# Kernel optimization log

Measured on AMD Instinct MI355X. Metric: run time of the kernel, lower is better.

The kernel has to match this reference:

```python
import jax, jax.numpy as jnp
import numpy as np

N_HEAD = 16
LN_EPS = 1e-5


def setup_inputs() -> dict:
    key = jax.random.key(0)
    ks = jax.random.split(key, 12)
    B, S, D = 4, 1024, 1024
    s = 1.0 / np.sqrt(D)
    return {
        "Q": jax.random.normal(ks[0], (B, S, D), jnp.float32),
        "K": jax.random.normal(ks[1], (B, S, D), jnp.float32),
        "V": jax.random.normal(ks[2], (B, S, D), jnp.float32),
        # Linear weights stored torch-style [out, in]
        "Wq": jax.random.normal(ks[3], (D, D), jnp.float32) * s,
        "bq": jnp.zeros((D,), jnp.float32),
        "Wk": jax.random.normal(ks[4], (D, D), jnp.float32) * s,
        "bk": jnp.zeros((D,), jnp.float32),
        "Wv": jax.random.normal(ks[5], (D, D), jnp.float32) * s,
        "bv": jnp.zeros((D,), jnp.float32),
        "Wo": jax.random.normal(ks[6], (D, D), jnp.float32) * s,
        "bo": jnp.zeros((D,), jnp.float32),
        "ln_g": jnp.ones((D,), jnp.float32),
        "ln_b": jnp.zeros((D,), jnp.float32),
    }


def _layer_norm(x, g, b):
    mu = jnp.mean(x, axis=-1, keepdims=True)
    var = jnp.mean(jnp.square(x - mu), axis=-1, keepdims=True)
    return (x - mu) * jax.lax.rsqrt(var + LN_EPS) * g + b


def reference(Q, K, V, Wq, bq, Wk, bk, Wv, bv, Wo, bo, ln_g, ln_b):
    B, S, D = Q.shape
    H = N_HEAD
    dk = D // H
    # projections, split heads: [B, H, S, dk]
    q = (Q @ Wq.T + bq).reshape(B, S, H, dk).transpose(0, 2, 1, 3)
    k = (K @ Wk.T + bk).reshape(B, S, H, dk).transpose(0, 2, 1, 3)
    v = (V @ Wv.T + bv).reshape(B, S, H, dk).transpose(0, 2, 1, 3)
    scores = jnp.einsum("bhqd,bhkd->bhqk", q, k) / np.sqrt(dk)
    # NOTE: original module applies softmax twice (F.softmax then nn.Softmax)
    attn = jax.nn.softmax(jax.nn.softmax(scores, axis=-1), axis=-1)
    ctx = jnp.einsum("bhqk,bhkd->bhqd", attn, v)  # [B, H, S, dk]
    ctx = ctx.transpose(0, 2, 1, 3).reshape(B, S, D)
    out = ctx @ Wo.T + bo
    return _layer_norm(out + Q, ln_g, ln_b)
```

## Files before the change

### kernel.cpp

```cpp
#include <hip/hip_runtime.h>
#include <cstdint>
#include <cstddef>


typedef unsigned short ushort_t;
typedef __attribute__((ext_vector_type(8))) short bf16x8;
typedef __attribute__((ext_vector_type(8))) unsigned short us8;
typedef __attribute__((ext_vector_type(4))) unsigned short us4;
typedef __attribute__((ext_vector_type(4))) float f32x4;

#define MFMA16(a, b, c) __builtin_amdgcn_mfma_f32_16x16x32_bf16((a), (b), (c), 0, 0, 0)
#define EXP2F(x) __builtin_amdgcn_exp2f(x)
#define LOG2E 1.4426950408889634f

__device__ __forceinline__ float b2f(ushort_t u) {
  union { unsigned int i; float f; } x; x.i = ((unsigned int)u) << 16; return x.f;
}
__device__ __forceinline__ ushort_t f2b(float f) {
  union { unsigned int i; float f; } x; x.f = f;
  unsigned int r = (x.i + 0x7FFFu + ((x.i >> 16) & 1u)) >> 16;
  return (ushort_t)r;
}
__device__ __forceinline__ us8 cvt8(float4 a, float4 b) {
  us8 r;
  r[0] = f2b(a.x); r[1] = f2b(a.y); r[2] = f2b(a.z); r[3] = f2b(a.w);
  r[4] = f2b(b.x); r[5] = f2b(b.y); r[6] = f2b(b.z); r[7] = f2b(b.w);
  return r;
}

__device__ __forceinline__ void gll16(const ushort_t* g, ushort_t* l) {
  __builtin_amdgcn_global_load_lds(
      (const __attribute__((address_space(1))) void*)g,
      (__attribute__((address_space(3))) void*)l, 16, 0, 0);
}

__global__ __launch_bounds__(256, 8) void cvt4_kernel(
    const float* __restrict__ w0, const float* __restrict__ w1,
    const float* __restrict__ w2, const float* __restrict__ w3,
    ushort_t* __restrict__ dst) {
  const int which = blockIdx.y;
  const float* src = (which == 0) ? w0 : (which == 1) ? w1 : (which == 2) ? w2 : w3;
  const int i = (blockIdx.x * 256 + threadIdx.x) * 8;
  const float4 a = *(const float4*)(src + i);
  const float4 b = *(const float4*)(src + i + 4);
  *(us8*)(dst + (size_t)which * 1048576 + i) = cvt8(a, b);
}

__global__ __launch_bounds__(256, 3) void qkv_proj_kernel(
    const float* __restrict__ Qin, const float* __restrict__ Kin,
    const float* __restrict__ Vin,
    const ushort_t* __restrict__ wq, const ushort_t* __restrict__ wk,
    const ushort_t* __restrict__ wv,
    const float* __restrict__ bq, const float* __restrict__ bk,
    const float* __restrict__ bv,
    ushort_t* __restrict__ qb, ushort_t* __restrict__ kb,
    ushort_t* __restrict__ vb) {
  __shared__ __align__(16) ushort_t Asl0[128 * 32];
  __shared__ __align__(16) ushort_t Asl1[128 * 32];
  __shared__ __align__(16) ushort_t Bsl0[128 * 32];
  __shared__ __align__(16) ushort_t Bsl1[128 * 32];
  const float* A; const ushort_t* W; const float* bias; float scale;
  if (blockIdx.z == 0)      { A = Qin; W = wq; bias = bq; scale = 0.125f * LOG2E; }
  else if (blockIdx.z == 1) { A = Kin; W = wk; bias = bk; scale = 1.0f; }
  else                      { A = Vin; W = wv; bias = bv; scale = 1.0f; }
  const int l = blockIdx.x;
  const int xcd = l & 7, ii = l >> 3;
  const int m0 = (xcd * 4 + (ii >> 3)) * 128;
  const int n0 = (ii & 7) * 128;
  const int tid = threadIdx.x;
  const int wave = tid >> 6, lane = tid & 63;
  const int l15 = lane & 15, quad = lane >> 4;
  const int wr = wave >> 1, wc = wave & 1;

  const int ra = tid >> 2, ca = (tid & 3) * 8;
  const float* Ap0 = A + (size_t)(m0 + ra) * 1024 + ca;
  const float* Ap1 = A + (size_t)(m0 + ra + 64) * 1024 + ca;

  const ushort_t* Bg0 = W + (size_t)(n0 + wave * 32 + (lane >> 2)) * 1024 + (lane & 3) * 8;
  const ushort_t* Bg1 = W + (size_t)(n0 + wave * 32 + 16 + (lane >> 2)) * 1024 + (lane & 3) * 8;

  float4 xa0 = *(const float4*)(Ap0), xa1 = *(const float4*)(Ap0 + 4);
  float4 xa2 = *(const float4*)(Ap1), xa3 = *(const float4*)(Ap1 + 4);
  gll16(Bg0, Bsl0 + wave * 1024);
  gll16(Bg1, Bsl0 + wave * 1024 + 512);
  *(us8*)(Asl0 + ra * 32 + ca) = cvt8(xa0, xa1);
  *(us8*)(Asl0 + (ra + 64) * 32 + ca) = cvt8(xa2, xa3);
  float4 ya0 = *(const float4*)(Ap0 + 32), ya1 = *(const float4*)(Ap0 + 36);
  float4 ya2 = *(const float4*)(Ap1 + 32), ya3 = *(const float4*)(Ap1 + 36);
  __syncthreads();

  f32x4 acc[4][4] = {};
#define QKV_COMPUTE(ASL, BSL)                                                   \
  {                                                                             \
    bf16x8 af[4], bfr[4];                                                       \
    _Pragma("unroll") for (int s = 0; s < 4; ++s)                               \
        af[s] = *(const bf16x8*)((ASL) + (wr * 64 + s * 16 + l15) * 32 + quad * 8); \
    _Pragma("unroll") for (int s = 0; s < 4; ++s)                               \
        bfr[s] = *(const bf16x8*)((BSL) + (wc * 64 + s * 16 + l15) * 32 + quad * 8); \
    _Pragma("unroll") for (int ms = 0; ms < 4; ++ms)                            \
        _Pragma("unroll") for (int ns = 0; ns < 4; ++ns)                        \
            acc[ms][ns] = MFMA16(af[ms], bfr[ns], acc[ms][ns]);                 \
  }

  for (int k0 = 0; k0 < 1024; k0 += 64) {
    {
      gll16(Bg0 + k0 + 32, Bsl1 + wave * 1024);
      gll16(Bg1 + k0 + 32, Bsl1 + wave * 1024 + 512);
      *(us8*)(Asl1 + ra * 32 + ca) = cvt8(ya0, ya1);
      *(us8*)(Asl1 + (ra + 64) * 32 + ca) = cvt8(ya2, ya3);
    }
    if (k0 + 64 < 1024) {
      xa0 = *(const float4*)(Ap0 + k0 + 64); xa1 = *(const float4*)(Ap0 + k0 + 68);
      xa2 = *(const float4*)(Ap1 + k0 + 64); xa3 = *(const float4*)(Ap1 + k0 + 68);
    }
    QKV_COMPUTE(Asl0, Bsl0)
    __syncthreads();
    if (k0 + 64 < 1024) {
      gll16(Bg0 + k0 + 64, Bsl0 + wave * 1024);
      gll16(Bg1 + k0 + 64, Bsl0 + wave * 1024 + 512);
      *(us8*)(Asl0 + ra * 32 + ca) = cvt8(xa0, xa1);
      *(us8*)(Asl0 + (ra + 64) * 32 + ca) = cvt8(xa2, xa3);
      if (k0 + 96 < 1024) {
        ya0 = *(const float4*)(Ap0 + k0 + 96); ya1 = *(const float4*)(Ap0 + k0 + 100);
        ya2 = *(const float4*)(Ap1 + k0 + 96); ya3 = *(const float4*)(Ap1 + k0 + 100);
      }
    }
    QKV_COMPUTE(Asl1, Bsl1)
    __syncthreads();
  }
#undef QKV_COMPUTE

  if (blockIdx.z != 2) {
    ushort_t* outp = (blockIdx.z == 0) ? qb : kb;
#pragma unroll
    for (int ns = 0; ns < 4; ++ns) {
      const int col = n0 + wc * 64 + ns * 16 + l15;
      const float bv_ = bias[col];
#pragma unroll
      for (int ms = 0; ms < 4; ++ms) {
        const int rowb = m0 + wr * 64 + ms * 16 + quad * 4;
#pragma unroll
        for (int r = 0; r < 4; ++r) {
          outp[(size_t)(rowb + r) * 1024 + col] =
              f2b((acc[ms][ns][r] + bv_) * scale);
        }
      }
    }
  } else {
#pragma unroll
    for (int ns = 0; ns < 4; ++ns) {
      const int col = n0 + wc * 64 + ns * 16 + l15;
      const float bv_ = bias[col];
      const int h = col >> 6, d = col & 63;
#pragma unroll
      for (int ms = 0; ms < 4; ++ms) {
        const int i0 = m0 + wr * 64 + ms * 16 + quad * 4;
        const int b = i0 >> 10, s0 = i0 & 1023;
        us4 pack;
#pragma unroll
        for (int r = 0; r < 4; ++r) pack[r] = f2b(acc[ms][ns][r] + bv_);
        *(us4*)(vb + ((size_t)(b * 16 + h) * 64 + d) * 1024 + s0) = pack;
      }
    }
  }
}

__global__ __launch_bounds__(256, 4) void attn_kernel(
    const ushort_t* __restrict__ qb, const ushort_t* __restrict__ kb,
    const ushort_t* __restrict__ vb, ushort_t* __restrict__ ctx) {
  __shared__ __align__(16) ushort_t Qs[64 * 72];
  __shared__ __align__(16) ushort_t Ks[64 * 72];
  __shared__ __align__(16) ushort_t Vt[64 * 72];
  __shared__ __align__(16) ushort_t Ps[4][16 * 68];

  const int tid = threadIdx.x, wave = tid >> 6, lane = tid & 63;
  const int l15 = lane & 15, quad = lane >> 4;
  const int l = blockIdx.x;
  const int xcd = l & 7, ii = l >> 3;
  const int bh = xcd * 8 + (ii >> 4);
  const int q0 = (ii & 15) * 64;
  const int b = bh >> 4, h = bh & 15;
  const ushort_t* qg = qb + ((size_t)b << 20) + h * 64;
  const ushort_t* kg = kb + ((size_t)b << 20) + h * 64;
  const ushort_t* vg = vb + ((size_t)bh << 16);

  const int kr0 = tid >> 3, kc0 = (tid & 7) * 8;
  const int kr1 = (tid + 256) >> 3, kc1 = kc0;

  *(us8*)(Qs + kr0 * 72 + kc0) = *(const us8*)(qg + (size_t)(q0 + kr0) * 1024 + kc0);
  *(us8*)(Qs + kr1 * 72 + kc1) = *(const us8*)(qg + (size_t)(q0 + kr1) * 1024 + kc1);
  __syncthreads();
  bf16x8 aqh[2];
  aqh[0] = *(const bf16x8*)(Qs + (wave * 16 + l15) * 72 + quad * 8);
  aqh[1] = *(const bf16x8*)(Qs + (wave * 16 + l15) * 72 + 32 + quad * 8);

  float z1[4] = {0.f, 0.f, 0.f, 0.f};
  us8 rk0 = *(const us8*)(kg + (size_t)kr0 * 1024 + kc0);
  us8 rk1 = *(const us8*)(kg + (size_t)kr1 * 1024 + kc1);
  for (int kt = 0; kt < 16; ++kt) {
    __syncthreads();
    *(us8*)(Ks + kr0 * 72 + kc0) = rk0;
    *(us8*)(Ks + kr1 * 72 + kc1) = rk1;
    __syncthreads();
    if (kt < 15) {
      rk0 = *(const us8*)(kg + (size_t)((kt + 1) * 64 + kr0) * 1024 + kc0);
      rk1 = *(const us8*)(kg + (size_t)((kt + 1) * 64 + kr1) * 1024 + kc1);
    }
    f32x4 sc[4] = {};
#pragma unroll
    for (int kk = 0; kk < 2; ++kk) {
#pragma unroll
      for (int ns = 0; ns < 4; ++ns) {
        const bf16x8 bk_ = *(const bf16x8*)(Ks + (ns * 16 + l15) * 72 + kk * 32 + quad * 8);
        sc[ns] = MFMA16(aqh[kk], bk_, sc[ns]);
      }
    }
#pragma unroll
    for (int ns = 0; ns < 4; ++ns)
#pragma unroll
      for (int r = 0; r < 4; ++r) z1[r] += EXP2F(sc[ns][r]);
  }
  float iz1[4];
#pragma unroll
  for (int r = 0; r < 4; ++r) {
    float s = z1[r];
#pragma unroll
    for (int off = 1; off < 16; off <<= 1) s += __shfl_xor(s, off, 64);
    iz1[r] = LOG2E / s;
  }

  f32x4 oac[4] = {};
  float z2[4] = {0.f, 0.f, 0.f, 0.f};
  rk0 = *(const us8*)(kg + (size_t)kr0 * 1024 + kc0);
  rk1 = *(const us8*)(kg + (size_t)kr1 * 1024 + kc1);
  us8 rv0 = *(const us8*)(vg + (size_t)kr0 * 1024 + kc0);
  us8 rv1 = *(const us8*)(vg + (size_t)kr1 * 1024 + kc1);
  for (int kt = 0; kt < 16; ++kt) {
    __syncthreads();
    *(us8*)(Ks + kr0 * 72 + kc0) = rk0;
    *(us8*)(Ks + kr1 * 72 + kc1) = rk1;
    *(us8*)(Vt + kr0 * 72 + kc0) = rv0;
    *(us8*)(Vt + kr1 * 72 + kc1) = rv1;
    __syncthreads();
    if (kt < 15) {
      rk0 = *(const us8*)(kg + (size_t)((kt + 1) * 64 + kr0) * 1024 + kc0);
      rk1 = *(const us8*)(kg + (size_t)((kt + 1) * 64 + kr1) * 1024 + kc1);
      rv0 = *(const us8*)(vg + (size_t)kr0 * 1024 + (kt + 1) * 64 + kc0);
      rv1 = *(const us8*)(vg + (size_t)kr1 * 1024 + (kt + 1) * 64 + kc1);
    }
    f32x4 sc[4] = {};
#pragma unroll
    for (int kk = 0; kk < 2; ++kk) {
#pragma unroll
      for (int ns = 0; ns < 4; ++ns) {
        const bf16x8 bk_ = *(const bf16x8*)(Ks + (ns * 16 + l15) * 72 + kk * 32 + quad * 8);
        sc[ns] = MFMA16(aqh[kk], bk_, sc[ns]);
      }
    }
#pragma unroll
    for (int ns = 0; ns < 4; ++ns)
#pragma unroll
      for (int r = 0; r < 4; ++r) {
        const float p1 = EXP2F(sc[ns][r]) * iz1[r];
        const float e2 = EXP2F(p1);
        z2[r] += e2;
        Ps[wave][(quad * 4 + r) * 68 + ns * 16 + l15] = f2b(e2);
      }
    __asm__ __volatile__("s_waitcnt lgkmcnt(0)" ::: "memory");
#pragma unroll
    for (int kk = 0; kk < 2; ++kk) {
      const ushort_t* pp = &Ps[wave][l15 * 68 + kk * 32 + quad * 8];
      union { us4 hseg[2]; bf16x8 v; } u;
      u.hseg[0] = *(const us4*)pp;
      u.hseg[1] = *(const us4*)(pp + 4);
      const bf16x8 ap = u.v;
#pragma unroll
      for (int ns2 = 0; ns2 < 4; ++ns2) {
        const bf16x8 bv_ = *(const bf16x8*)(Vt + (ns2 * 16 + l15) * 72 + kk * 32 + quad * 8);
        oac[ns2] = MFMA16(ap, bv_, oac[ns2]);
      }
    }
  }

#pragma unroll
  for (int r = 0; r < 4; ++r) {
    float s = z2[r];
#pragma unroll
    for (int off = 1; off < 16; off <<= 1) s += __shfl_xor(s, off, 64);
    z2[r] = s;
  }
#pragma unroll
  for (int ns2 = 0; ns2 < 4; ++ns2) {
    const int d = ns2 * 16 + l15;
#pragma unroll
    for (int r = 0; r < 4; ++r) {
      const int s = q0 + wave * 16 + quad * 4 + r;
      ctx[((size_t)(b * 1024 + s)) * 1024 + h * 64 + d] = f2b(oac[ns2][r] / z2[r]);
    }
  }
}

__global__ __launch_bounds__(256, 4) void out_proj_kernel(
    const ushort_t* __restrict__ ctxp, const ushort_t* __restrict__ wo,
    const float* __restrict__ bo, ushort_t* __restrict__ pre) {
  __shared__ __align__(16) ushort_t Asl0[64 * 32];
  __shared__ __align__(16) ushort_t Asl1[64 * 32];
  __shared__ __align__(16) ushort_t Bsl0[128 * 32];
  __shared__ __align__(16) ushort_t Bsl1[128 * 32];
  const int tid = threadIdx.x;
  const int wave = tid >> 6, lane = tid & 63;
  const int l15 = lane & 15, quad = lane >> 4;
  const int wr = wave >> 1, wc = wave & 1;
  const int l = blockIdx.x;
  const int xcd = l & 7, ii = l >> 3;
  const int m0 = (xcd * 8 + (ii >> 3)) * 64;
  const int n0 = (ii & 7) * 128;

  const ushort_t* Ag = ctxp + (size_t)(m0 + wave * 16 + (lane >> 2)) * 1024 + (lane & 3) * 8;
  const ushort_t* Bg0 = wo + (size_t)(n0 + wave * 32 + (lane >> 2)) * 1024 + (lane & 3) * 8;
  const ushort_t* Bg1 = wo + (size_t)(n0 + wave * 32 + 16 + (lane >> 2)) * 1024 + (lane & 3) * 8;

  gll16(Ag, Asl0 + wave * 512);
  gll16(Bg0, Bsl0 + wave * 1024);
  gll16(Bg1, Bsl0 + wave * 1024 + 512);
  __syncthreads();

  f32x4 acc[2][4] = {};
#define OUTP_COMPUTE(ASL, BSL)                                                  \
  {                                                                             \
    bf16x8 af[2], bfr[4];                                                       \
    _Pragma("unroll") for (int s = 0; s < 2; ++s)                               \
        af[s] = *(const bf16x8*)((ASL) + (wr * 32 + s * 16 + l15) * 32 + quad * 8); \
    _Pragma("unroll") for (int s = 0; s < 4; ++s)                               \
        bfr[s] = *(const bf16x8*)((BSL) + (wc * 64 + s * 16 + l15) * 32 + quad * 8); \
    _Pragma("unroll") for (int ms = 0; ms < 2; ++ms)                            \
        _Pragma("unroll") for (int ns = 0; ns < 4; ++ns)                        \
            acc[ms][ns] = MFMA16(af[ms], bfr[ns], acc[ms][ns]);                 \
  }

  for (int k0 = 0; k0 < 1024; k0 += 64) {
    {
      gll16(Ag + k0 + 32, Asl1 + wave * 512);
      gll16(Bg0 + k0 + 32, Bsl1 + wave * 1024);
      gll16(Bg1 + k0 + 32, Bsl1 + wave * 1024 + 512);
    }
    OUTP_COMPUTE(Asl0, Bsl0)
    __syncthreads();
    if (k0 + 64 < 1024) {
      gll16(Ag + k0 + 64, Asl0 + wave * 512);
      gll16(Bg0 + k0 + 64, Bsl0 + wave * 1024);
      gll16(Bg1 + k0 + 64, Bsl0 + wave * 1024 + 512);
    }
    OUTP_COMPUTE(Asl1, Bsl1)
    __syncthreads();
  }
#undef OUTP_COMPUTE

#pragma unroll
  for (int ns = 0; ns < 4; ++ns) {
    const int col = n0 + wc * 64 + ns * 16 + l15;
    const float bv_ = bo[col];
#pragma unroll
    for (int ms = 0; ms < 2; ++ms) {
      const int rowb = m0 + wr * 32 + ms * 16 + quad * 4;
#pragma unroll
      for (int r = 0; r < 4; ++r) {
        pre[(size_t)(rowb + r) * 1024 + col] = f2b(acc[ms][ns][r] + bv_);
      }
    }
  }
}

__global__ __launch_bounds__(256, 4) void ln_kernel(
    const ushort_t* __restrict__ pre, const float* __restrict__ Q,
    const float* __restrict__ g, const float* __restrict__ bta,
    float* __restrict__ out) {
  const int row = blockIdx.x;
  const int tid = threadIdx.x;
  const size_t base = (size_t)row * 1024 + tid * 4;
  const ushort4 p4 = *(const ushort4*)(pre + base);
  const float4 q4 = *(const float4*)(Q + base);
  float v[4] = {b2f(p4.x) + q4.x, b2f(p4.y) + q4.y,
                b2f(p4.z) + q4.z, b2f(p4.w) + q4.w};
  float s1 = v[0] + v[1] + v[2] + v[3];
  float s2 = v[0]*v[0] + v[1]*v[1] + v[2]*v[2] + v[3]*v[3];
#pragma unroll
  for (int off = 1; off < 64; off <<= 1) {
    s1 += __shfl_xor(s1, off, 64);
    s2 += __shfl_xor(s2, off, 64);
  }
  __shared__ float r1[4], r2[4];
  const int wave = tid >> 6, lane = tid & 63;
  if (lane == 0) { r1[wave] = s1; r2[wave] = s2; }
  __syncthreads();
  const float t1 = r1[0] + r1[1] + r1[2] + r1[3];
  const float t2 = r2[0] + r2[1] + r2[2] + r2[3];
  const float mu = t1 * (1.0f / 1024.0f);
  const float var = t2 * (1.0f / 1024.0f) - mu * mu;
  const float inv = rsqrtf(var + 1e-5f);
  const int c0 = tid * 4;
#pragma unroll
  for (int j = 0; j < 4; ++j) {
    const int c = c0 + j;
    out[(size_t)row * 1024 + c] = (v[j] - mu) * inv * g[c] + bta[c];
  }
}

extern "C" void kernel_launch(void* const* d_in, const int* in_sizes, int n_in,
                              void* d_out, int out_size, void* d_ws, size_t ws_size,
                              hipStream_t stream) {
  const float* Q  = (const float*)d_in[0];
  const float* K  = (const float*)d_in[1];
  const float* V  = (const float*)d_in[2];
  const float* Wq = (const float*)d_in[3];
  const float* bq = (const float*)d_in[4];
  const float* Wk = (const float*)d_in[5];
  const float* bk = (const float*)d_in[6];
  const float* Wv = (const float*)d_in[7];
  const float* bv = (const float*)d_in[8];
  const float* Wo = (const float*)d_in[9];
  const float* bo = (const float*)d_in[10];
  const float* lg = (const float*)d_in[11];
  const float* lb = (const float*)d_in[12];

  char* ws = (char*)d_ws;
  ushort_t* qb  = (ushort_t*)(ws);
  ushort_t* kb  = (ushort_t*)(ws + ((size_t)8  << 20));
  ushort_t* vb  = (ushort_t*)(ws + ((size_t)16 << 20));
  ushort_t* pre = (ushort_t*)(ws);

  ushort_t* dptr  = (ushort_t*)d_out;
  ushort_t* wo_bf = dptr;
  ushort_t* wq_bf = dptr + 1048576;
  ushort_t* wk_bf = dptr + 2097152;
  ushort_t* wv_bf = dptr + 3145728;
  ushort_t* ctx   = dptr + 4194304;
  float*    out   = (float*)d_out;

  cvt4_kernel<<<dim3(512, 4), 256, 0, stream>>>(Wo, Wq, Wk, Wv, dptr);
  qkv_proj_kernel<<<dim3(256, 1, 3), 256, 0, stream>>>(Q, K, V, wq_bf, wk_bf, wv_bf,
                                                       bq, bk, bv, qb, kb, vb);
  attn_kernel<<<dim3(1024), 256, 0, stream>>>(qb, kb, vb, ctx);
  out_proj_kernel<<<dim3(512), 256, 0, stream>>>(ctx, wo_bf, bo, pre);
  ln_kernel<<<dim3(4096), 256, 0, stream>>>(pre, Q, lg, lb, out);
}
```

Before: 240.1 us.

## Load QKV A operand directly to registers and keep attention P in registers

The QKV projection now loads fp32 activations straight into per-lane MFMA fragment layout and converts them with packed bf16 conversion instructions, which drops the A-tile LDS staging and uses explicit vmcnt waits with raw barriers. The attention kernel swaps MFMA operand order so each lane holds a full query row. The softmax probabilities are then passed to the PV MFMA through ds_bpermute instead of a round trip through LDS, and the reductions and context stores are vectorized. The aim is to cut LDS traffic, barrier cost and per-element conversions, at the price of uncoalesced global loads for A and trickier wait-count bookkeeping.

```diff
diff --git a/kernel.cpp b/kernel.cpp
--- a/kernel.cpp
+++ b/kernel.cpp
@@ -26,6 +26,17 @@
   r[0] = f2b(a.x); r[1] = f2b(a.y); r[2] = f2b(a.z); r[3] = f2b(a.w);
   r[4] = f2b(b.x); r[5] = f2b(b.y); r[6] = f2b(b.z); r[7] = f2b(b.w);
   return r;
+}
+__device__ __forceinline__ unsigned int cvtpk(float lo, float hi) {
+  unsigned int r;
+  asm("v_cvt_pk_bf16_f32 %0, %1, %2" : "=v"(r) : "v"(lo), "v"(hi));
+  return r;
+}
+__device__ __forceinline__ bf16x8 cvt8pk(float4 a, float4 b) {
+  union { unsigned int u[4]; bf16x8 v; } r;
+  r.u[0] = cvtpk(a.x, a.y); r.u[1] = cvtpk(a.z, a.w);
+  r.u[2] = cvtpk(b.x, b.y); r.u[3] = cvtpk(b.z, b.w);
+  return r.v;
 }
 
 __device__ __forceinline__ void gll16(const ushort_t* g, ushort_t* l) {
@@ -55,8 +66,6 @@
     const float* __restrict__ bv,
     ushort_t* __restrict__ qb, ushort_t* __restrict__ kb,
     ushort_t* __restrict__ vb) {
-  __shared__ __align__(16) ushort_t Asl0[128 * 32];
-  __shared__ __align__(16) ushort_t Asl1[128 * 32];
   __shared__ __align__(16) ushort_t Bsl0[128 * 32];
   __shared__ __align__(16) ushort_t Bsl1[128 * 32];
   const float* A; const ushort_t* W; const float* bias; float scale;
@@ -72,63 +81,78 @@
   const int l15 = lane & 15, quad = lane >> 4;
   const int wr = wave >> 1, wc = wave & 1;
 
-  const int ra = tid >> 2, ca = (tid & 3) * 8;
-  const float* Ap0 = A + (size_t)(m0 + ra) * 1024 + ca;
-  const float* Ap1 = A + (size_t)(m0 + ra + 64) * 1024 + ca;
+  const float* Ap[4];
+#pragma unroll
+  for (int s = 0; s < 4; ++s)
+    Ap[s] = A + (size_t)(m0 + wr * 64 + s * 16 + l15) * 1024 + quad * 8;
 
   const ushort_t* Bg0 = W + (size_t)(n0 + wave * 32 + (lane >> 2)) * 1024 + (lane & 3) * 8;
   const ushort_t* Bg1 = W + (size_t)(n0 + wave * 32 + 16 + (lane >> 2)) * 1024 + (lane & 3) * 8;
-
-  float4 xa0 = *(const float4*)(Ap0), xa1 = *(const float4*)(Ap0 + 4);
-  float4 xa2 = *(const float4*)(Ap1), xa3 = *(const float4*)(Ap1 + 4);
-  gll16(Bg0, Bsl0 + wave * 1024);
-  gll16(Bg1, Bsl0 + wave * 1024 + 512);
-  *(us8*)(Asl0 + ra * 32 + ca) = cvt8(xa0, xa1);
-  *(us8*)(Asl0 + (ra + 64) * 32 + ca) = cvt8(xa2, xa3);
-  float4 ya0 = *(const float4*)(Ap0 + 32), ya1 = *(const float4*)(Ap0 + 36);
-  float4 ya2 = *(const float4*)(Ap1 + 32), ya3 = *(const float4*)(Ap1 + 36);
-  __syncthreads();
+  ushort_t* Bl0a = Bsl0 + wave * 1024; ushort_t* Bl0b = Bl0a + 512;
+  ushort_t* Bl1a = Bsl1 + wave * 1024; ushort_t* Bl1b = Bl1a + 512;
+
+  float4 X[4][2], Y[4][2];
+#pragma unroll
+  for (int s = 0; s < 4; ++s) { X[s][0] = *(const float4*)(Ap[s]); X[s][1] = *(const float4*)(Ap[s] + 4); }
+  gll16(Bg0, Bl0a);
+  gll16(Bg1, Bl0b);
+#pragma unroll
+  for (int s = 0; s < 4; ++s) { Y[s][0] = *(const float4*)(Ap[s] + 32); Y[s][1] = *(const float4*)(Ap[s] + 36); }
+  asm volatile("s_waitcnt vmcnt(8)" ::: "memory");
+  __builtin_amdgcn_s_barrier();
 
   f32x4 acc[4][4] = {};
-#define QKV_COMPUTE(ASL, BSL)                                                   \
+#define QKV_MFMA(AFR, BSL)                                                      \
   {                                                                             \
-    bf16x8 af[4], bfr[4];                                                       \
-    _Pragma("unroll") for (int s = 0; s < 4; ++s)                               \
-        af[s] = *(const bf16x8*)((ASL) + (wr * 64 + s * 16 + l15) * 32 + quad * 8); \
+    bf16x8 bfr[4];                                                              \
     _Pragma("unroll") for (int s = 0; s < 4; ++s)                               \
         bfr[s] = *(const bf16x8*)((BSL) + (wc * 64 + s * 16 + l15) * 32 + quad * 8); \
     _Pragma("unroll") for (int ms = 0; ms < 4; ++ms)                            \
         _Pragma("unroll") for (int ns = 0; ns < 4; ++ns)                        \
-            acc[ms][ns] = MFMA16(af[ms], bfr[ns], acc[ms][ns]);                 \
+            acc[ms][ns] = MFMA16((AFR)[ms], bfr[ns], acc[ms][ns]);              \
   }
 
   for (int k0 = 0; k0 < 1024; k0 += 64) {
+    gll16(Bg0 + k0 + 32, Bl1a);
+    gll16(Bg1 + k0 + 32, Bl1b);
     {
-      gll16(Bg0 + k0 + 32, Bsl1 + wave * 1024);
-      gll16(Bg1 + k0 + 32, Bsl1 + wave * 1024 + 512);
-      *(us8*)(Asl1 + ra * 32 + ca) = cvt8(ya0, ya1);
-      *(us8*)(Asl1 + (ra + 64) * 32 + ca) = cvt8(ya2, ya3);
-    }
+      bf16x8 af[4];
+#pragma unroll
+      for (int s = 0; s < 4; ++s) af[s] = cvt8pk(X[s][0], X[s][1]);
+      if (k0 + 64 < 1024) {
+#pragma unroll
+        for (int s = 0; s < 4; ++s) {
+          X[s][0] = *(const float4*)(Ap[s] + k0 + 64);
+          X[s][1] = *(const float4*)(Ap[s] + k0 + 68);
+        }
+      }
+      QKV_MFMA(af, Bsl0)
+    }
+    if (k0 + 64 < 1024) asm volatile("s_waitcnt vmcnt(8)" ::: "memory");
+    else                asm volatile("s_waitcnt vmcnt(0)" ::: "memory");
+    __builtin_amdgcn_s_barrier();
     if (k0 + 64 < 1024) {
-      xa0 = *(const float4*)(Ap0 + k0 + 64); xa1 = *(const float4*)(Ap0 + k0 + 68);
-      xa2 = *(const float4*)(Ap1 + k0 + 64); xa3 = *(const float4*)(Ap1 + k0 + 68);
-    }
-    QKV_COMPUTE(Asl0, Bsl0)
-    __syncthreads();
-    if (k0 + 64 < 1024) {
-      gll16(Bg0 + k0 + 64, Bsl0 + wave * 1024);
-      gll16(Bg1 + k0 + 64, Bsl0 + wave * 1024 + 512);
-      *(us8*)(Asl0 + ra * 32 + ca) = cvt8(xa0, xa1);
-      *(us8*)(Asl0 + (ra + 64) * 32 + ca) = cvt8(xa2, xa3);
+      gll16(Bg0 + k0 + 64, Bl0a);
+      gll16(Bg1 + k0 + 64, Bl0b);
+    }
+    {
+      bf16x8 af[4];
+#pragma unroll
+      for (int s = 0; s < 4; ++s) af[s] = cvt8pk(Y[s][0], Y[s][1]);
       if (k0 + 96 < 1024) {
-        ya0 = *(const float4*)(Ap0 + k0 + 96); ya1 = *(const float4*)(Ap0 + k0 + 100);
-        ya2 = *(const float4*)(Ap1 + k0 + 96); ya3 = *(const float4*)(Ap1 + k0 + 100);
-      }
-    }
-    QKV_COMPUTE(Asl1, Bsl1)
-    __syncthreads();
-  }
-#undef QKV_COMPUTE
+#pragma unroll
+        for (int s = 0; s < 4; ++s) {
+          Y[s][0] = *(const float4*)(Ap[s] + k0 + 96);
+          Y[s][1] = *(const float4*)(Ap[s] + k0 + 100);
+        }
+      }
+      QKV_MFMA(af, Bsl1)
+    }
+    if (k0 + 96 < 1024) asm volatile("s_waitcnt vmcnt(8)" ::: "memory");
+    else                asm volatile("s_waitcnt vmcnt(0)" ::: "memory");
+    __builtin_amdgcn_s_barrier();
+  }
+#undef QKV_MFMA
 
   if (blockIdx.z != 2) {
     ushort_t* outp = (blockIdx.z == 0) ? qb : kb;
@@ -171,7 +195,6 @@
   __shared__ __align__(16) ushort_t Qs[64 * 72];
   __shared__ __align__(16) ushort_t Ks[64 * 72];
   __shared__ __align__(16) ushort_t Vt[64 * 72];
-  __shared__ __align__(16) ushort_t Ps[4][16 * 68];
 
   const int tid = threadIdx.x, wave = tid >> 6, lane = tid & 63;
   const int l15 = lane & 15, quad = lane >> 4;
@@ -194,7 +217,7 @@
   aqh[0] = *(const bf16x8*)(Qs + (wave * 16 + l15) * 72 + quad * 8);
   aqh[1] = *(const bf16x8*)(Qs + (wave * 16 + l15) * 72 + 32 + quad * 8);
 
-  float z1[4] = {0.f, 0.f, 0.f, 0.f};
+  float z1 = 0.f;
   us8 rk0 = *(const us8*)(kg + (size_t)kr0 * 1024 + kc0);
   us8 rk1 = *(const us8*)(kg + (size_t)kr1 * 1024 + kc1);
   for (int kt = 0; kt < 16; ++kt) {
@@ -211,26 +234,24 @@
     for (int kk = 0; kk < 2; ++kk) {
 #pragma unroll
       for (int ns = 0; ns < 4; ++ns) {
-        const bf16x8 bk_ = *(const bf16x8*)(Ks + (ns * 16 + l15) * 72 + kk * 32 + quad * 8);
-        sc[ns] = MFMA16(aqh[kk], bk_, sc[ns]);
+        const bf16x8 kf = *(const bf16x8*)(Ks + (ns * 16 + l15) * 72 + kk * 32 + quad * 8);
+        sc[ns] = MFMA16(kf, aqh[kk], sc[ns]);
       }
     }
 #pragma unroll
     for (int ns = 0; ns < 4; ++ns)
 #pragma unroll
-      for (int r = 0; r < 4; ++r) z1[r] += EXP2F(sc[ns][r]);
-  }
-  float iz1[4];
-#pragma unroll
-  for (int r = 0; r < 4; ++r) {
-    float s = z1[r];
-#pragma unroll
-    for (int off = 1; off < 16; off <<= 1) s += __shfl_xor(s, off, 64);
-    iz1[r] = LOG2E / s;
-  }
+      for (int r = 0; r < 4; ++r) z1 += EXP2F(sc[ns][r]);
+  }
+  z1 += __shfl_xor(z1, 16, 64);
+  z1 += __shfl_xor(z1, 32, 64);
+  const float iz1 = LOG2E / z1;
+
+  const int adr0 = ((((quad & 1) << 1) * 16) + l15) << 2;
+  const int adr1 = adr0 + 64;
 
   f32x4 oac[4] = {};
-  float z2[4] = {0.f, 0.f, 0.f, 0.f};
+  float z2 = 0.f;
   rk0 = *(const us8*)(kg + (size_t)kr0 * 1024 + kc0);
   rk1 = *(const us8*)(kg + (size_t)kr1 * 1024 + kc1);
   us8 rv0 = *(const us8*)(vg + (size_t)kr0 * 1024 + kc0);
@@ -253,50 +274,49 @@
     for (int kk = 0; kk < 2; ++kk) {
 #pragma unroll
       for (int ns = 0; ns < 4; ++ns) {
-        const bf16x8 bk_ = *(const bf16x8*)(Ks + (ns * 16 + l15) * 72 + kk * 32 + quad * 8);
-        sc[ns] = MFMA16(aqh[kk], bk_, sc[ns]);
-      }
-    }
-#pragma unroll
-    for (int ns = 0; ns < 4; ++ns)
-#pragma unroll
-      for (int r = 0; r < 4; ++r) {
-        const float p1 = EXP2F(sc[ns][r]) * iz1[r];
-        const float e2 = EXP2F(p1);
-        z2[r] += e2;
-        Ps[wave][(quad * 4 + r) * 68 + ns * 16 + l15] = f2b(e2);
-      }
-    __asm__ __volatile__("s_waitcnt lgkmcnt(0)" ::: "memory");
+        const bf16x8 kf = *(const bf16x8*)(Ks + (ns * 16 + l15) * 72 + kk * 32 + quad * 8);
+        sc[ns] = MFMA16(kf, aqh[kk], sc[ns]);
+      }
+    }
+    unsigned int D[4][2];
+#pragma unroll
+    for (int ns = 0; ns < 4; ++ns) {
+      const float e0 = EXP2F(EXP2F(sc[ns][0]) * iz1);
+      const float e1 = EXP2F(EXP2F(sc[ns][1]) * iz1);
+      const float e2 = EXP2F(EXP2F(sc[ns][2]) * iz1);
+      const float e3 = EXP2F(EXP2F(sc[ns][3]) * iz1);
+      z2 += (e0 + e1) + (e2 + e3);
+      D[ns][0] = cvtpk(e0, e1);
+      D[ns][1] = cvtpk(e2, e3);
+    }
 #pragma unroll
     for (int kk = 0; kk < 2; ++kk) {
-      const ushort_t* pp = &Ps[wave][l15 * 68 + kk * 32 + quad * 8];
-      union { us4 hseg[2]; bf16x8 v; } u;
-      u.hseg[0] = *(const us4*)pp;
-      u.hseg[1] = *(const us4*)(pp + 4);
-      const bf16x8 ap = u.v;
+      union { unsigned int u[4]; bf16x8 v; } pf;
+#pragma unroll
+      for (int t = 0; t < 4; ++t) {
+        const int adr = (t >> 1) ? adr1 : adr0;
+        const int lo = __builtin_amdgcn_ds_bpermute(adr, (int)D[2 * kk][t & 1]);
+        const int hi = __builtin_amdgcn_ds_bpermute(adr, (int)D[2 * kk + 1][t & 1]);
+        pf.u[t] = (unsigned int)((quad >= 2) ? hi : lo);
+      }
 #pragma unroll
       for (int ns2 = 0; ns2 < 4; ++ns2) {
-        const bf16x8 bv_ = *(const bf16x8*)(Vt + (ns2 * 16 + l15) * 72 + kk * 32 + quad * 8);
-        oac[ns2] = MFMA16(ap, bv_, oac[ns2]);
-      }
-    }
-  }
-
-#pragma unroll
-  for (int r = 0; r < 4; ++r) {
-    float s = z2[r];
-#pragma unroll
-    for (int off = 1; off < 16; off <<= 1) s += __shfl_xor(s, off, 64);
-    z2[r] = s;
-  }
+        const bf16x8 vf = *(const bf16x8*)(Vt + (ns2 * 16 + l15) * 72 + kk * 32 + quad * 8);
+        oac[ns2] = MFMA16(vf, pf.v, oac[ns2]);
+      }
+    }
+  }
+
+  z2 += __shfl_xor(z2, 16, 64);
+  z2 += __shfl_xor(z2, 32, 64);
+  const int s = q0 + wave * 16 + l15;
+  ushort_t* crow = ctx + ((size_t)(b * 1024 + s)) * 1024 + h * 64;
 #pragma unroll
   for (int ns2 = 0; ns2 < 4; ++ns2) {
-    const int d = ns2 * 16 + l15;
-#pragma unroll
-    for (int r = 0; r < 4; ++r) {
-      const int s = q0 + wave * 16 + quad * 4 + r;
-      ctx[((size_t)(b * 1024 + s)) * 1024 + h * 64 + d] = f2b(oac[ns2][r] / z2[r]);
-    }
+    us4 pack;
+#pragma unroll
+    for (int r = 0; r < 4; ++r) pack[r] = f2b(oac[ns2][r] / z2);
+    *(us4*)(crow + ns2 * 16 + quad * 4) = pack;
   }
 }
 
```

Measured after the change: 338.9 us. +41.2%, slower.
